# Optimization experiments

Measured on AMD Instinct MI355X. Metric: run time of the kernel, lower is better.

Reference implementation:

```python
import jax, jax.numpy as jnp
import numpy as np

H = 4096      # hidden_size (also vocab size of the embedding, per source)
O = 4096      # output_size (also embedding dim, per source)
MAX_LEN = 15


def setup_inputs() -> dict:
    key = jax.random.key(0)
    ks = jax.random.split(key, 16)
    s = 0.02  # init scale
    inp = {
        "input_ids": jax.random.randint(ks[0], (1,), 0, H),
        "hidden": jax.random.normal(ks[1], (1, 1, H), jnp.float32),
        "e_output": jax.random.normal(ks[2], (1, H), jnp.float32),   # unused, kept for signature fidelity
        "e_output_seq": jax.random.normal(ks[3], (MAX_LEN, H), jnp.float32),
        # parameters
        "emb_W": jax.random.normal(ks[4], (H, O), jnp.float32) * s,
        "att_W": jax.random.normal(ks[5], (MAX_LEN, H + O), jnp.float32) * s,
        "att_b": jnp.zeros((MAX_LEN,), jnp.float32),
        "comb_W": jax.random.normal(ks[6], (H, H + O), jnp.float32) * s,
        "comb_b": jnp.zeros((H,), jnp.float32),
        "gru_W_ih": jax.random.normal(ks[7], (3 * H, H), jnp.float32) * s,
        "gru_W_hh": jax.random.normal(ks[8], (3 * H, H), jnp.float32) * s,
        "gru_b_ih": jnp.zeros((3 * H,), jnp.float32),
        "gru_b_hh": jnp.zeros((3 * H,), jnp.float32),
        "out_W": jax.random.normal(ks[9], (O, H), jnp.float32) * s,
        "out_b": jnp.zeros((O,), jnp.float32),
    }
    return inp


def reference(input_ids, hidden, e_output, e_output_seq, emb_W, att_W, att_b,
              comb_W, comb_b, gru_W_ih, gru_W_hh, gru_b_ih, gru_b_hh, out_W, out_b):
    # dropout is identity in eval mode
    emb = emb_W[input_ids[0]][None, :]                       # [1, O]
    h0 = hidden[0]                                            # [1, H]
    att_logits = jnp.concatenate([emb, h0], axis=1) @ att_W.T + att_b
    att_weights = jax.nn.softmax(att_logits, axis=-1)         # [1, MAX_LEN]
    att_applied = att_weights @ e_output_seq                   # [1, H]
    combined = jnp.concatenate([emb, att_applied], axis=1)     # [1, H+O]
    x = jax.nn.relu(combined @ comb_W.T + comb_b)              # [1, H]
    # GRU cell (PyTorch gate order: r, z, n)
    gi = x @ gru_W_ih.T + gru_b_ih                             # [1, 3H]
    gh = h0 @ gru_W_hh.T + gru_b_hh                            # [1, 3H]
    i_r, i_z, i_n = jnp.split(gi, 3, axis=1)
    h_r, h_z, h_n = jnp.split(gh, 3, axis=1)
    r = jax.nn.sigmoid(i_r + h_r)
    z = jax.nn.sigmoid(i_z + h_z)
    n = jnp.tanh(i_n + r * h_n)
    h_new = (1.0 - z) * n + z * h0                             # [1, H]
    out = jax.nn.log_softmax(h_new @ out_W.T + out_b, axis=-1)  # [1, O]
    return out, h_new[None, :, :], att_weights
```

## Files before the change

### kernel.cpp

```cpp
#include <hip/hip_runtime.h>

#define H 4096
#define O 4096
#define HO 8192
#define MAXLEN 15
#define CHUNK 256

typedef const __attribute__((address_space(1))) unsigned int* as1_u32p;
typedef __attribute__((address_space(3))) unsigned int* as3_u32p;

__device__ __forceinline__ void stage1k(const float* g, float* l) {
    __builtin_amdgcn_global_load_lds((as1_u32p)g, (as3_u32p)l, 16, 0, 0);
}

#define WAITV(N) asm volatile("s_waitcnt vmcnt(" #N ")" ::: "memory")
#define REGION_FENCE() do { asm volatile("" ::: "memory"); __builtin_amdgcn_sched_barrier(0); } while (0)

__device__ __forceinline__ void mv2(const float* __restrict__ W, int row, int K, int NC,
                                    const float* __restrict__ x, float* sst, int lane,
                                    float& out0, float& out1) {
    const float* wr0 = W + (size_t)row * K;
    const float* wr1 = wr0 + K;
    stage1k(wr0 + lane * 4, sst);
    stage1k(wr1 + lane * 4, sst + CHUNK);
    float4 xcur = *(const float4*)(x + lane * 4);
    REGION_FENCE();
    float acc0 = 0.f, acc1 = 0.f;
    for (int t = 0; t < NC; ++t) {
        float4 xnext = xcur;
        if (t + 1 < NC) {
            const int b = ((t + 1) & 1) * (2 * CHUNK);
            stage1k(wr0 + (size_t)(t + 1) * CHUNK + lane * 4, sst + b);
            stage1k(wr1 + (size_t)(t + 1) * CHUNK + lane * 4, sst + b + CHUNK);
            xnext = *(const float4*)(x + (size_t)(t + 1) * CHUNK + lane * 4);
            WAITV(3);
        } else {
            WAITV(0);
        }
        __builtin_amdgcn_sched_barrier(0);
        const int rb = (t & 1) * (2 * CHUNK);
        float4 a  = *(const float4*)(sst + rb + lane * 4);
        float4 b4 = *(const float4*)(sst + rb + CHUNK + lane * 4);
        acc0 += a.x  * xcur.x + a.y  * xcur.y + a.z  * xcur.z + a.w  * xcur.w;
        acc1 += b4.x * xcur.x + b4.y * xcur.y + b4.z * xcur.z + b4.w * xcur.w;
        xcur = xnext;
    }
    #pragma unroll
    for (int off = 32; off; off >>= 1) {
        acc0 += __shfl_down(acc0, off, 64);
        acc1 += __shfl_down(acc1, off, 64);
    }
    out0 = acc0; out1 = acc1;
}

__global__ __launch_bounds__(1024) void k_attlogit(const int* __restrict__ ids,
                                                   const float* __restrict__ hidden,
                                                   const float* __restrict__ embW,
                                                   const float* __restrict__ attW,
                                                   const float* __restrict__ attb,
                                                   float* __restrict__ attlog) {
    __shared__ float sred[16];
    const int tid = threadIdx.x, lane = tid & 63, wave = tid >> 6;
    const int j = blockIdx.x;
    const float* emb = embW + (size_t)ids[0] * O;
    const float4* w4 = (const float4*)(attW + (size_t)j * (H + O));
    const float4* e4 = (const float4*)emb;
    const float4* h4 = (const float4*)hidden;

    float4 wv0 = w4[tid];
    float4 xv0 = e4[tid];
    float4 wv1 = w4[tid + 1024];
    float4 xv1 = h4[tid];
    float acc = wv0.x * xv0.x + wv0.y * xv0.y + wv0.z * xv0.z + wv0.w * xv0.w
              + wv1.x * xv1.x + wv1.y * xv1.y + wv1.z * xv1.z + wv1.w * xv1.w;
    #pragma unroll
    for (int off = 32; off; off >>= 1) acc += __shfl_down(acc, off, 64);
    if (lane == 0) sred[wave] = acc;
    __syncthreads();
    if (tid == 0) {
        float s = 0.f;
        #pragma unroll
        for (int w = 0; w < 16; w++) s += sred[w];
        attlog[j] = s + attb[j];
    }
}

__global__ __launch_bounds__(256) void k_attapply(const int* __restrict__ ids,
                                                  const float* __restrict__ embW,
                                                  const float* __restrict__ attlog,
                                                  const float* __restrict__ eseq,
                                                  float* __restrict__ combined,
                                                  float* __restrict__ out_attw) {
    const int k = blockIdx.x * 256 + threadIdx.x;
    float l[MAXLEN];
    float m = -1e30f;
    #pragma unroll
    for (int j = 0; j < MAXLEN; j++) { l[j] = attlog[j]; m = fmaxf(m, l[j]); }
    float s = 0.f;
    #pragma unroll
    for (int j = 0; j < MAXLEN; j++) { l[j] = __expf(l[j] - m); s += l[j]; }
    const float inv = 1.f / s;

    float acc = 0.f;
    #pragma unroll
    for (int j = 0; j < MAXLEN; j++) acc += l[j] * eseq[j * H + k];
    combined[O + k] = acc * inv;
    combined[k] = embW[(size_t)ids[0] * O + k];
    if (blockIdx.x == 0 && threadIdx.x < MAXLEN) out_attw[threadIdx.x] = l[threadIdx.x] * inv;
}

__global__ __launch_bounds__(512) void k_mvA(const float* __restrict__ combW,
                                             const float* __restrict__ combB,
                                             const float* __restrict__ ghhW,
                                             const float* __restrict__ ghhB,
                                             const float* __restrict__ hidden,
                                             const float* __restrict__ combined,
                                             float* __restrict__ xout,
                                             float* __restrict__ ghout) {
    __shared__ __align__(16) float sst[8 * 4 * CHUNK];
    const int wave = threadIdx.x >> 6, lane = threadIdx.x & 63;
    float* st = sst + wave * 4 * CHUNK;
    float r0, r1;
    if (wave < 2) {
        const int row = blockIdx.x * 4 + wave * 2;
        mv2(combW, row, HO, HO / CHUNK, combined, st, lane, r0, r1);
        if (lane == 0) {
            xout[row]     = fmaxf(r0 + combB[row], 0.f);
            xout[row + 1] = fmaxf(r1 + combB[row + 1], 0.f);
        }
    } else {
        const int row = blockIdx.x * 12 + (wave - 2) * 2;
        mv2(ghhW, row, H, H / CHUNK, hidden, st, lane, r0, r1);
        if (lane == 0) {
            ghout[row]     = r0 + ghhB[row];
            ghout[row + 1] = r1 + ghhB[row + 1];
        }
    }
}

__global__ __launch_bounds__(512) void k_mvB(const float* __restrict__ gihW,
                                             const float* __restrict__ gihB,
                                             const float* __restrict__ x,
                                             float* __restrict__ giout) {
    __shared__ __align__(16) float sst[8 * 4 * CHUNK];
    const int wave = threadIdx.x >> 6, lane = threadIdx.x & 63;
    float* st = sst + wave * 4 * CHUNK;
    const int row = blockIdx.x * 16 + wave * 2;
    float r0, r1;
    mv2(gihW, row, H, H / CHUNK, x, st, lane, r0, r1);
    if (lane == 0) {
        giout[row]     = r0 + gihB[row];
        giout[row + 1] = r1 + gihB[row + 1];
    }
}

__global__ __launch_bounds__(256) void k_gate(const float* __restrict__ gi,
                                              const float* __restrict__ gh,
                                              const float* __restrict__ hidden,
                                              float* __restrict__ hout,
                                              float* __restrict__ out_h) {
    const int i = blockIdx.x * 256 + threadIdx.x;
    float r = 1.f / (1.f + __expf(-(gi[i] + gh[i])));
    float z = 1.f / (1.f + __expf(-(gi[i + H] + gh[i + H])));
    float n = tanhf(gi[i + 2 * H] + r * gh[i + 2 * H]);
    float h = (1.f - z) * n + z * hidden[i];
    hout[i] = h;
    out_h[i] = h;
}

__global__ __launch_bounds__(512) void k_mvC(const float* __restrict__ outW,
                                             const float* __restrict__ outB,
                                             const float* __restrict__ h,
                                             float* __restrict__ logits) {
    __shared__ __align__(16) float sst[8 * 4 * CHUNK];
    const int wave = threadIdx.x >> 6, lane = threadIdx.x & 63;
    float* st = sst + wave * 4 * CHUNK;
    const int row = blockIdx.x * 16 + wave * 2;
    float r0, r1;
    mv2(outW, row, H, H / CHUNK, h, st, lane, r0, r1);
    if (lane == 0) {
        logits[row]     = r0 + outB[row];
        logits[row + 1] = r1 + outB[row + 1];
    }
}

__global__ __launch_bounds__(1024) void k_lsm(const float* __restrict__ logits,
                                              float* __restrict__ out) {
    __shared__ float red[16];
    __shared__ float red2[16];
    const int tid = threadIdx.x, lane = tid & 63, wave = tid >> 6;
    float m = -1e30f;
    for (int k = tid; k < O; k += 1024) m = fmaxf(m, logits[k]);
    #pragma unroll
    for (int off = 32; off; off >>= 1) m = fmaxf(m, __shfl_down(m, off, 64));
    if (lane == 0) red[wave] = m;
    __syncthreads();
    if (tid == 0) {
        float mm = -1e30f;
        for (int j = 0; j < 16; j++) mm = fmaxf(mm, red[j]);
        red[0] = mm;
    }
    __syncthreads();
    m = red[0];
    float s = 0.f;
    for (int k = tid; k < O; k += 1024) s += __expf(logits[k] - m);
    #pragma unroll
    for (int off = 32; off; off >>= 1) s += __shfl_down(s, off, 64);
    if (lane == 0) red2[wave] = s;
    __syncthreads();
    if (tid == 0) {
        float ss = 0.f;
        for (int j = 0; j < 16; j++) ss += red2[j];
        red2[0] = m + logf(ss);
    }
    __syncthreads();
    float lse = red2[0];
    for (int k = tid; k < O; k += 1024) out[k] = logits[k] - lse;
}

extern "C" void kernel_launch(void* const* d_in, const int* in_sizes, int n_in,
                              void* d_out, int out_size, void* d_ws, size_t ws_size,
                              hipStream_t stream) {
    const int*   ids    = (const int*)d_in[0];
    const float* hidden = (const float*)d_in[1];
    const float* eseq   = (const float*)d_in[3];
    const float* embW   = (const float*)d_in[4];
    const float* attW   = (const float*)d_in[5];
    const float* attb   = (const float*)d_in[6];
    const float* combW  = (const float*)d_in[7];
    const float* combB  = (const float*)d_in[8];
    const float* gihW   = (const float*)d_in[9];
    const float* ghhW   = (const float*)d_in[10];
    const float* gihB   = (const float*)d_in[11];
    const float* ghhB   = (const float*)d_in[12];
    const float* outW   = (const float*)d_in[13];
    const float* outB   = (const float*)d_in[14];
    float* out = (float*)d_out;

    float* ws       = (float*)d_ws;
    float* combined = ws;
    float* xbuf     = ws + 8192;
    float* ghbuf    = ws + 12288;
    float* gibuf    = ws + 24576;
    float* hbuf     = ws + 36864;
    float* logits   = ws + 40960;
    float* attlog   = ws + 45056;

    k_attlogit<<<MAXLEN, 1024, 0, stream>>>(ids, hidden, embW, attW, attb, attlog);
    k_attapply<<<16,     256,  0, stream>>>(ids, embW, attlog, eseq, combined, out + 8192);
    k_mvA     <<<1024,   512,  0, stream>>>(combW, combB, ghhW, ghhB, hidden, combined, xbuf, ghbuf);
    k_mvB     <<<768,    512,  0, stream>>>(gihW, gihB, xbuf, gibuf);
    k_gate    <<<16,     256,  0, stream>>>(gibuf, ghbuf, hidden, hbuf, out + 4096);
    k_mvC     <<<256,    512,  0, stream>>>(outW, outB, hbuf, logits);
    k_lsm     <<<1,      1024, 0, stream>>>(logits, out);
}
```

Before: 575.5 us.

## Replace LDS-staged per-wave GEMV with register-resident x, multi-row blocks

```diff
diff --git a/kernel.cpp b/kernel.cpp
--- a/kernel.cpp
+++ b/kernel.cpp
@@ -4,53 +4,48 @@
 #define O 4096
 #define HO 8192
 #define MAXLEN 15
-#define CHUNK 256
-
-typedef const __attribute__((address_space(1))) unsigned int* as1_u32p;
-typedef __attribute__((address_space(3))) unsigned int* as3_u32p;
-
-__device__ __forceinline__ void stage1k(const float* g, float* l) {
-    __builtin_amdgcn_global_load_lds((as1_u32p)g, (as3_u32p)l, 16, 0, 0);
-}
-
-#define WAITV(N) asm volatile("s_waitcnt vmcnt(" #N ")" ::: "memory")
-#define REGION_FENCE() do { asm volatile("" ::: "memory"); __builtin_amdgcn_sched_barrier(0); } while (0)
-
-__device__ __forceinline__ void mv2(const float* __restrict__ W, int row, int K, int NC,
-                                    const float* __restrict__ x, float* sst, int lane,
-                                    float& out0, float& out1) {
-    const float* wr0 = W + (size_t)row * K;
-    const float* wr1 = wr0 + K;
-    stage1k(wr0 + lane * 4, sst);
-    stage1k(wr1 + lane * 4, sst + CHUNK);
-    float4 xcur = *(const float4*)(x + lane * 4);
-    REGION_FENCE();
-    float acc0 = 0.f, acc1 = 0.f;
-    for (int t = 0; t < NC; ++t) {
-        float4 xnext = xcur;
-        if (t + 1 < NC) {
-            const int b = ((t + 1) & 1) * (2 * CHUNK);
-            stage1k(wr0 + (size_t)(t + 1) * CHUNK + lane * 4, sst + b);
-            stage1k(wr1 + (size_t)(t + 1) * CHUNK + lane * 4, sst + b + CHUNK);
-            xnext = *(const float4*)(x + (size_t)(t + 1) * CHUNK + lane * 4);
-            WAITV(3);
-        } else {
-            WAITV(0);
-        }
-        __builtin_amdgcn_sched_barrier(0);
-        const int rb = (t & 1) * (2 * CHUNK);
-        float4 a  = *(const float4*)(sst + rb + lane * 4);
-        float4 b4 = *(const float4*)(sst + rb + CHUNK + lane * 4);
-        acc0 += a.x  * xcur.x + a.y  * xcur.y + a.z  * xcur.z + a.w  * xcur.w;
-        acc1 += b4.x * xcur.x + b4.y * xcur.y + b4.z * xcur.z + b4.w * xcur.w;
-        xcur = xnext;
-    }
-    #pragma unroll
-    for (int off = 32; off; off >>= 1) {
-        acc0 += __shfl_down(acc0, off, 64);
-        acc1 += __shfl_down(acc1, off, 64);
-    }
-    out0 = acc0; out1 = acc1;
+
+__device__ __forceinline__ float dot4f(const float4 a, const float4 b) {
+    return a.x * b.x + a.y * b.y + a.z * b.z + a.w * b.w;
+}
+
+#define XRED(v) { _Pragma("unroll") for (int o_ = 32; o_; o_ >>= 1) v += __shfl_xor(v, o_, 64); }
+
+template<int C, int R, bool RELU>
+__device__ __forceinline__ void gemv_rows(const float* __restrict__ W,
+                                          const float* __restrict__ x,
+                                          const float* __restrict__ bias,
+                                          float* __restrict__ y,
+                                          int row0) {
+    __shared__ float spart[4][R];
+    const int tid = threadIdx.x, lane = tid & 63, w = tid >> 6;
+    const int K4 = 256 * C;
+    const float4* x4 = (const float4*)x;
+    float4 xs[C];
+    #pragma unroll
+    for (int c = 0; c < C; c++) xs[c] = x4[w * (64 * C) + lane + 64 * c];
+
+    float acc[R];
+    const float4* Wr = (const float4*)W + (size_t)row0 * K4 + w * (64 * C) + lane;
+    #pragma unroll
+    for (int r = 0; r < R; r++) {
+        const float4* wrow = Wr + (size_t)r * K4;
+        float s = 0.f;
+        #pragma unroll
+        for (int c = 0; c < C; c++) s += dot4f(wrow[64 * c], xs[c]);
+        acc[r] = s;
+    }
+    #pragma unroll
+    for (int r = 0; r < R; r++) { XRED(acc[r]); }
+    if (lane == 0) {
+        #pragma unroll
+        for (int r = 0; r < R; r++) spart[w][r] = acc[r];
+    }
+    __syncthreads();
+    if (tid < R) {
+        float v = spart[0][tid] + spart[1][tid] + spart[2][tid] + spart[3][tid] + bias[row0 + tid];
+        y[row0 + tid] = RELU ? fmaxf(v, 0.f) : v;
+    }
 }
 
 __global__ __launch_bounds__(1024) void k_attlogit(const int* __restrict__ ids,
@@ -71,10 +66,8 @@
     float4 xv0 = e4[tid];
     float4 wv1 = w4[tid + 1024];
     float4 xv1 = h4[tid];
-    float acc = wv0.x * xv0.x + wv0.y * xv0.y + wv0.z * xv0.z + wv0.w * xv0.w
-              + wv1.x * xv1.x + wv1.y * xv1.y + wv1.z * xv1.z + wv1.w * xv1.w;
-    #pragma unroll
-    for (int off = 32; off; off >>= 1) acc += __shfl_down(acc, off, 64);
+    float acc = dot4f(wv0, xv0) + dot4f(wv1, xv1);
+    XRED(acc);
     if (lane == 0) sred[wave] = acc;
     __syncthreads();
     if (tid == 0) {
@@ -109,49 +102,32 @@
     if (blockIdx.x == 0 && threadIdx.x < MAXLEN) out_attw[threadIdx.x] = l[threadIdx.x] * inv;
 }
 
-__global__ __launch_bounds__(512) void k_mvA(const float* __restrict__ combW,
-                                             const float* __restrict__ combB,
-                                             const float* __restrict__ ghhW,
-                                             const float* __restrict__ ghhB,
-                                             const float* __restrict__ hidden,
-                                             const float* __restrict__ combined,
-                                             float* __restrict__ xout,
-                                             float* __restrict__ ghout) {
-    __shared__ __align__(16) float sst[8 * 4 * CHUNK];
-    const int wave = threadIdx.x >> 6, lane = threadIdx.x & 63;
-    float* st = sst + wave * 4 * CHUNK;
-    float r0, r1;
-    if (wave < 2) {
-        const int row = blockIdx.x * 4 + wave * 2;
-        mv2(combW, row, HO, HO / CHUNK, combined, st, lane, r0, r1);
-        if (lane == 0) {
-            xout[row]     = fmaxf(r0 + combB[row], 0.f);
-            xout[row + 1] = fmaxf(r1 + combB[row + 1], 0.f);
-        }
-    } else {
-        const int row = blockIdx.x * 12 + (wave - 2) * 2;
-        mv2(ghhW, row, H, H / CHUNK, hidden, st, lane, r0, r1);
-        if (lane == 0) {
-            ghout[row]     = r0 + ghhB[row];
-            ghout[row + 1] = r1 + ghhB[row + 1];
-        }
-    }
-}
-
-__global__ __launch_bounds__(512) void k_mvB(const float* __restrict__ gihW,
-                                             const float* __restrict__ gihB,
+__global__ __launch_bounds__(256) void k_ghh(const float* __restrict__ W,
+                                             const float* __restrict__ b,
                                              const float* __restrict__ x,
-                                             float* __restrict__ giout) {
-    __shared__ __align__(16) float sst[8 * 4 * CHUNK];
-    const int wave = threadIdx.x >> 6, lane = threadIdx.x & 63;
-    float* st = sst + wave * 4 * CHUNK;
-    const int row = blockIdx.x * 16 + wave * 2;
-    float r0, r1;
-    mv2(gihW, row, H, H / CHUNK, x, st, lane, r0, r1);
-    if (lane == 0) {
-        giout[row]     = r0 + gihB[row];
-        giout[row + 1] = r1 + gihB[row + 1];
-    }
+                                             float* __restrict__ y) {
+    gemv_rows<4, 16, false>(W, x, b, y, blockIdx.x * 16);
+}
+
+__global__ __launch_bounds__(256) void k_comb(const float* __restrict__ W,
+                                              const float* __restrict__ b,
+                                              const float* __restrict__ x,
+                                              float* __restrict__ y) {
+    gemv_rows<8, 8, true>(W, x, b, y, blockIdx.x * 8);
+}
+
+__global__ __launch_bounds__(256) void k_gih(const float* __restrict__ W,
+                                             const float* __restrict__ b,
+                                             const float* __restrict__ x,
+                                             float* __restrict__ y) {
+    gemv_rows<4, 16, false>(W, x, b, y, blockIdx.x * 16);
+}
+
+__global__ __launch_bounds__(256) void k_outw(const float* __restrict__ W,
+                                              const float* __restrict__ b,
+                                              const float* __restrict__ x,
+                                              float* __restrict__ y) {
+    gemv_rows<4, 8, false>(W, x, b, y, blockIdx.x * 8);
 }
 
 __global__ __launch_bounds__(256) void k_gate(const float* __restrict__ gi,
@@ -168,22 +144,6 @@
     out_h[i] = h;
 }
 
-__global__ __launch_bounds__(512) void k_mvC(const float* __restrict__ outW,
-                                             const float* __restrict__ outB,
-                                             const float* __restrict__ h,
-                                             float* __restrict__ logits) {
-    __shared__ __align__(16) float sst[8 * 4 * CHUNK];
-    const int wave = threadIdx.x >> 6, lane = threadIdx.x & 63;
-    float* st = sst + wave * 4 * CHUNK;
-    const int row = blockIdx.x * 16 + wave * 2;
-    float r0, r1;
-    mv2(outW, row, H, H / CHUNK, h, st, lane, r0, r1);
-    if (lane == 0) {
-        logits[row]     = r0 + outB[row];
-        logits[row + 1] = r1 + outB[row + 1];
-    }
-}
-
 __global__ __launch_bounds__(1024) void k_lsm(const float* __restrict__ logits,
                                               float* __restrict__ out) {
     __shared__ float red[16];
@@ -192,7 +152,7 @@
     float m = -1e30f;
     for (int k = tid; k < O; k += 1024) m = fmaxf(m, logits[k]);
     #pragma unroll
-    for (int off = 32; off; off >>= 1) m = fmaxf(m, __shfl_down(m, off, 64));
+    for (int off = 32; off; off >>= 1) m = fmaxf(m, __shfl_xor(m, off, 64));
     if (lane == 0) red[wave] = m;
     __syncthreads();
     if (tid == 0) {
@@ -204,8 +164,7 @@
     m = red[0];
     float s = 0.f;
     for (int k = tid; k < O; k += 1024) s += __expf(logits[k] - m);
-    #pragma unroll
-    for (int off = 32; off; off >>= 1) s += __shfl_down(s, off, 64);
+    XRED(s);
     if (lane == 0) red2[wave] = s;
     __syncthreads();
     if (tid == 0) {
@@ -248,9 +207,10 @@
 
     k_attlogit<<<MAXLEN, 1024, 0, stream>>>(ids, hidden, embW, attW, attb, attlog);
     k_attapply<<<16,     256,  0, stream>>>(ids, embW, attlog, eseq, combined, out + 8192);
-    k_mvA     <<<1024,   512,  0, stream>>>(combW, combB, ghhW, ghhB, hidden, combined, xbuf, ghbuf);
-    k_mvB     <<<768,    512,  0, stream>>>(gihW, gihB, xbuf, gibuf);
+    k_ghh     <<<768,    256,  0, stream>>>(ghhW, ghhB, hidden, ghbuf);
+    k_comb    <<<512,    256,  0, stream>>>(combW, combB, combined, xbuf);
+    k_gih     <<<768,    256,  0, stream>>>(gihW, gihB, xbuf, gibuf);
     k_gate    <<<16,     256,  0, stream>>>(gibuf, ghbuf, hidden, hbuf, out + 4096);
-    k_mvC     <<<256,    512,  0, stream>>>(outW, outB, hbuf, logits);
+    k_outw    <<<512,    256,  0, stream>>>(outW, outB, hbuf, logits);
     k_lsm     <<<1,      1024, 0, stream>>>(logits, out);
 }
```

Result: no change. 569.0 us (-1.1%).
